# Kernel optimization log

Hardware: AMD Instinct MI355X
Metric: run time of the kernel (lower is better)

Reference implementation:

```python
import jax, jax.numpy as jnp
import numpy as np

B, N, TAPS, T = 64, 2000, 64, 2000


def setup_inputs() -> dict:
    key = jax.random.key(0)
    k1, k2 = jax.random.split(key)
    return {
        "x_seq": jax.random.normal(k1, (B, N, TAPS), dtype=jnp.float32),
        "d_seq": jax.random.normal(k2, (B, N), dtype=jnp.float32),
        # one learnable forgetting factor per unrolled RLS layer, init 0.99
        "lambdas": jnp.full((T,), 0.99, dtype=jnp.float32),
    }


def reference(x_seq, d_seq, lambdas):
    Bb, Nn, taps = x_seq.shape
    steps = min(lambdas.shape[0], Nn)
    w0 = jnp.zeros((Bb, taps), dtype=x_seq.dtype)
    P0 = jnp.broadcast_to(jnp.eye(taps, dtype=x_seq.dtype), (Bb, taps, taps))

    # time-major inputs for lax.scan
    xs = (jnp.swapaxes(x_seq[:, :steps, :], 0, 1),  # (steps, B, taps)
          jnp.swapaxes(d_seq[:, :steps], 0, 1),     # (steps, B)
          lambdas[:steps])                           # (steps,)

    def step(carry, inp):
        w, P = carry
        x, d, lam = inp
        lam = jnp.clip(lam, 1e-4, 0.9999)
        Px = jnp.einsum('bij,bj->bi', P, x)                 # (B, taps)
        denom = lam + jnp.einsum('bi,bi->b', x, Px)          # (B,)
        g = Px / denom[:, None]                              # gain (B, taps)
        y_hat = jnp.sum(w * x, axis=-1)                      # (B,)
        w_next = w + g * (d - y_hat)[:, None]
        xP = jnp.einsum('bj,bjk->bk', x, P)                  # x^T P, (B, taps)
        P_next = (P - g[:, :, None] * xP[:, None, :]) / lam  # rank-1 downdate
        return (w_next, P_next), y_hat

    (w_final, P_final), y_hats = jax.lax.scan(step, (w0, P0), xs)
    return jnp.swapaxes(y_hats, 0, 1), w_final  # (B, steps), (B, taps)
```

## Files before the change

kernel.cpp:

```cpp
#include <hip/hip_runtime.h>


#define B_ 64
#define N_ 2000
#define TAPS_ 64
#define STEPS_ 2000
#define VST_ 72

typedef float f2 __attribute__((ext_vector_type(2)));

__device__ __forceinline__ f2 pk2(float v) { f2 r; r.x = v; r.y = v; return r; }

__device__ __forceinline__ void lds_barrier() {
    asm volatile("s_waitcnt lgkmcnt(0)\n\ts_barrier" ::: "memory");
}

__device__ __forceinline__ float clipl(float v) {
    return fminf(fmaxf(v, 1e-4f), 0.9999f);
}

__device__ __forceinline__ float quad_reduce(float v) {
    float r;
    asm("s_nop 1\n\t"
        "v_add_f32_dpp %0, %1, %1 quad_perm:[1,0,3,2] row_mask:0xf bank_mask:0xf\n\t"
        "s_nop 1\n\t"
        "v_add_f32_dpp %0, %0, %0 quad_perm:[2,3,0,1] row_mask:0xf bank_mask:0xf"
        : "=&v"(r) : "v"(v));
    return r;
}

__device__ __forceinline__ float rcp_nr(float v) {
    float r = __builtin_amdgcn_rcpf(v);
    float e = fmaf(-v, r, 1.0f);
    return fmaf(r, e, r);
}

__global__ __launch_bounds__(256, 1) void rls_kernel(
    const float* __restrict__ x_seq,
    const float* __restrict__ d_seq,
    const float* __restrict__ lambdas,
    float* __restrict__ y_out,
    float* __restrict__ w_out)
{
    const int b   = blockIdx.x;
    const int tid = threadIdx.x;
    const int r   = tid >> 2;
    const int q   = tid & 3;
    const int qb  = q << 4;

    __shared__ __align__(16) float  bufs[2][4][VST_];
    __shared__ __align__(16) float  d_lds[STEPS_];
    __shared__ __align__(16) float2 lam2[STEPS_];

    const float* xb = x_seq + (size_t)b * N_ * TAPS_;
    const float* db = d_seq + (size_t)b * N_;

    for (int idx = tid; idx < STEPS_; idx += 256) {
        d_lds[idx] = db[idx];
        const float lc = clipl(lambdas[idx]);
        lam2[idx] = make_float2(lc, rcp_nr(lc));
    }

    f2 Q[8], QT[8], w[8];
    #pragma unroll
    for (int j = 0; j < 8; ++j) {
        Q[j].x = (qb + 2*j     == r) ? 1.0f : 0.0f;
        Q[j].y = (qb + 2*j + 1 == r) ? 1.0f : 0.0f;
        QT[j] = Q[j];
        w[j]  = pk2(0.0f);
    }
    float sig = 1.0f;

    auto unpack4 = [](f2* dst, float4 v) {
        dst[0].x = v.x; dst[0].y = v.y; dst[1].x = v.z; dst[1].y = v.w;
    };

    auto loadpair = [&](f2 (&dA)[8], f2 (&dB)[8], int row) {
        const float4* v0 = (const float4*)(xb + (size_t)row * TAPS_ + qb);
        const float4* v1 = (const float4*)(xb + (size_t)(row + 1) * TAPS_ + qb);
        #pragma unroll
        for (int j4 = 0; j4 < 4; ++j4) {
            unpack4(&dA[2*j4], v0[j4]);
            unpack4(&dB[2*j4], v1[j4]);
        }
    };

    f2 P0a[8], P0b[8], P1a[8], P1b[8], P2a[8], P2b[8], P3a[8], P3b[8];
    loadpair(P0a, P0b, 0);
    loadpair(P1a, P1b, 2);
    loadpair(P2a, P2b, 4);

    float qxrS, xqrS, urS, vrS, wy0S, wy1S;

    {
        f2 qx2 = pk2(0.f), xq2 = pk2(0.f), u2 = pk2(0.f), v2 = pk2(0.f);
        #pragma unroll
        for (int j = 0; j < 8; ++j) {
            qx2 = __builtin_elementwise_fma(Q[j],  P0a[j], qx2);
            xq2 = __builtin_elementwise_fma(QT[j], P0a[j], xq2);
            u2  = __builtin_elementwise_fma(Q[j],  P0b[j], u2);
            v2  = __builtin_elementwise_fma(QT[j], P0b[j], v2);
        }
        qxrS = quad_reduce(qx2.x + qx2.y);
        xqrS = quad_reduce(xq2.x + xq2.y);
        urS  = quad_reduce(u2.x + u2.y);
        vrS  = quad_reduce(v2.x + v2.y);
        bufs[0][q][r] = (q == 0) ? qxrS : (q == 1) ? xqrS : (q == 2) ? urS : vrS;

        f2 wy02 = pk2(0.f), wy12 = pk2(0.f);
        #pragma unroll
        for (int j = 0; j < 8; ++j) {
            wy02 = __builtin_elementwise_fma(w[j], P0a[j], wy02);
            wy12 = __builtin_elementwise_fma(w[j], P0b[j], wy12);
        }
        wy0S = quad_reduce(wy02.x + wy02.y);
        wy1S = quad_reduce(wy12.x + wy12.y);
    }

    auto round = [&](int t, f2 (&x0)[8], f2 (&x1)[8],
                     f2 (&xn0)[8], f2 (&xn1)[8],
                     f2 (&xf0)[8], f2 (&xf1)[8],
                     int par, bool pf, bool fuse)
    {
        lds_barrier();

        f2 Qxq[8], xQq[8], uq[8], vq[8];
        {
            const float4* p0 = (const float4*)(&bufs[par][0][qb]);
            const float4* p1 = (const float4*)(&bufs[par][1][qb]);
            #pragma unroll
            for (int j4 = 0; j4 < 4; ++j4) {
                unpack4(&Qxq[2*j4], p0[j4]);
                unpack4(&xQq[2*j4], p1[j4]);
            }
            const float4* p2 = (const float4*)(&bufs[par][2][qb]);
            const float4* p3 = (const float4*)(&bufs[par][3][qb]);
            #pragma unroll
            for (int j4 = 0; j4 < 4; ++j4) {
                unpack4(&uq[2*j4], p2[j4]);
                unpack4(&vq[2*j4], p3[j4]);
            }
        }
        const float4 lf = *(const float4*)&lam2[t];
        const float2 dd = *(const float2*)&d_lds[t];

        if (pf) loadpair(xf0, xf1, t + 6);

        f2 pd2 = pk2(0.f);
        #pragma unroll
        for (int j = 0; j < 8; ++j)
            pd2 = __builtin_elementwise_fma(x0[j], Qxq[j], pd2);
        const float pd0  = quad_reduce(pd2.x + pd2.y);
        const float den0 = fmaf(sig, pd0, lf.x);
        const float s0   = sig * rcp_nr(den0);

        f2 a2 = pk2(0.f), bb2 = pk2(0.f);
        #pragma unroll
        for (int j = 0; j < 8; ++j) {
            a2  = __builtin_elementwise_fma(x1[j], xQq[j], a2);
            bb2 = __builtin_elementwise_fma(x1[j], Qxq[j], bb2);
        }
        const float a  = quad_reduce(a2.x + a2.y);
        const float bb = quad_reduce(bb2.x + bb2.y);

        f2 c22 = pk2(0.f);
        #pragma unroll
        for (int j = 0; j < 8; ++j)
            c22 = __builtin_elementwise_fma(x1[j], uq[j], c22);
        const float c2 = quad_reduce(c22.x + c22.y);

        const float err0 = dd.x - wy0S;
        const float es0  = s0 * err0;
        const float sa   = s0 * a;
        const float sb   = s0 * bb;

        const float sig1 = sig * lf.y;
        const float pd1  = fmaf(-sa, bb, c2);
        const float den1 = fmaf(sig1, pd1, lf.z);
        const float s1   = sig1 * rcp_nr(den1);
        const float y1   = fmaf(es0, bb, wy1S);
        const float err1 = dd.y - y1;
        const float es1  = s1 * err1;
        sig = sig1 * lf.w;

        if (tid == 0)
            *(float2*)(y_out + (size_t)b * N_ + t) = make_float2(wy0S, y1);

        const float qx1r = fmaf(-sa, qxrS, urS);
        const float xq1r = fmaf(-sb, xqrS, vrS);
        const f2 nsa   = pk2(-sa);
        const f2 nsb   = pk2(-sb);
        const f2 s0v   = pk2(s0);
        const f2 s1v   = pk2(s1);
        const f2 es0v  = pk2(es0);
        const f2 es1v  = pk2(es1);
        const f2 ntr0  = pk2(-(s0 * qxrS));
        const f2 ntr1  = pk2(-(s1 * qx1r));
        const f2 nxqr  = pk2(-xqrS);
        const f2 nxq1r = pk2(-xq1r);

        f2 nqx = pk2(0.f), nxq = pk2(0.f), nu = pk2(0.f), nv = pk2(0.f);
        f2 nw0 = pk2(0.f), nw1 = pk2(0.f);

        #pragma unroll
        for (int j = 0; j < 8; ++j) {
            const f2 Qx1 = __builtin_elementwise_fma(nsa, Qxq[j], uq[j]);
            const f2 xQ1 = __builtin_elementwise_fma(nsb, xQq[j], vq[j]);
            const f2 tq0 = s0v * Qxq[j];
            const f2 tq1 = s1v * Qx1;
            w[j] = __builtin_elementwise_fma(Qxq[j], es0v, w[j]);
            w[j] = __builtin_elementwise_fma(Qx1,    es1v, w[j]);
            Q[j] = __builtin_elementwise_fma(ntr0, xQq[j], Q[j]);
            Q[j] = __builtin_elementwise_fma(ntr1, xQ1,    Q[j]);
            QT[j] = __builtin_elementwise_fma(tq0, nxqr,  QT[j]);
            QT[j] = __builtin_elementwise_fma(tq1, nxq1r, QT[j]);
            if (fuse) {
                nqx = __builtin_elementwise_fma(Q[j],  xn0[j], nqx);
                nxq = __builtin_elementwise_fma(QT[j], xn0[j], nxq);
                nu  = __builtin_elementwise_fma(Q[j],  xn1[j], nu);
                nv  = __builtin_elementwise_fma(QT[j], xn1[j], nv);
                nw0 = __builtin_elementwise_fma(w[j],  xn0[j], nw0);
                nw1 = __builtin_elementwise_fma(w[j],  xn1[j], nw1);
            }
        }

        if (fuse) {
            qxrS = quad_reduce(nqx.x + nqx.y);
            xqrS = quad_reduce(nxq.x + nxq.y);
            urS  = quad_reduce(nu.x + nu.y);
            vrS  = quad_reduce(nv.x + nv.y);
            bufs[par ^ 1][q][r] =
                (q == 0) ? qxrS : (q == 1) ? xqrS : (q == 2) ? urS : vrS;
            wy0S = quad_reduce(nw0.x + nw0.y);
            wy1S = quad_reduce(nw1.x + nw1.y);
        }
    };

    for (int t = 0; t < 1992; t += 8) {
        round(t + 0, P0a, P0b, P1a, P1b, P3a, P3b, 0, true, true);
        round(t + 2, P1a, P1b, P2a, P2b, P0a, P0b, 1, true, true);
        round(t + 4, P2a, P2b, P3a, P3b, P1a, P1b, 0, true, true);
        round(t + 6, P3a, P3b, P0a, P0b, P2a, P2b, 1, true, true);
    }
    round(1992, P0a, P0b, P1a, P1b, P3a, P3b, 0, true,  true);
    round(1994, P1a, P1b, P2a, P2b, P0a, P0b, 1, false, true);
    round(1996, P2a, P2b, P3a, P3b, P1a, P1b, 0, false, true);
    round(1998, P3a, P3b, P0a, P0b, P2a, P2b, 1, false, false);

    if (r == 0) {
        float4* wo = (float4*)(w_out + (size_t)b * TAPS_ + qb);
        #pragma unroll
        for (int j4 = 0; j4 < 4; ++j4)
            wo[j4] = make_float4(w[2*j4].x, w[2*j4].y, w[2*j4+1].x, w[2*j4+1].y);
    }
}

extern "C" void kernel_launch(void* const* d_in, const int* in_sizes, int n_in,
                              void* d_out, int out_size, void* d_ws, size_t ws_size,
                              hipStream_t stream) {
    const float* x_seq   = (const float*)d_in[0];
    const float* d_seq   = (const float*)d_in[1];
    const float* lambdas = (const float*)d_in[2];

    float* y_out = (float*)d_out;
    float* w_out = (float*)d_out + (size_t)B_ * N_;

    rls_kernel<<<B_, 256, 0, stream>>>(x_seq, d_seq, lambdas, y_out, w_out);
}
```

Measured before the change: 900.4 us.

## Block four RLS time steps per barrier round instead of two

Extends the blocked rank-update scheme from two to four steps per round. The small Gram-like dot products among the four input vectors are computed serially and the four rank-1 updates of Q, QT and w are applied together. This halves the number of LDS barriers and exchange rounds per sequence. In exchange, each round carries more serial scalar dependency work and much higher register pressure, and the prefetch distance drops to one quad ahead.

```diff
diff --git a/kernel.cpp b/kernel.cpp
--- a/kernel.cpp
+++ b/kernel.cpp
@@ -48,7 +48,7 @@
     const int q   = tid & 3;
     const int qb  = q << 4;
 
-    __shared__ __align__(16) float  bufs[2][4][VST_];
+    __shared__ __align__(16) float  bufs[2][8][VST_];
     __shared__ __align__(16) float  d_lds[STEPS_];
     __shared__ __align__(16) float2 lam2[STEPS_];
 
@@ -75,177 +75,241 @@
         dst[0].x = v.x; dst[0].y = v.y; dst[1].x = v.z; dst[1].y = v.w;
     };
 
-    auto loadpair = [&](f2 (&dA)[8], f2 (&dB)[8], int row) {
-        const float4* v0 = (const float4*)(xb + (size_t)row * TAPS_ + qb);
-        const float4* v1 = (const float4*)(xb + (size_t)(row + 1) * TAPS_ + qb);
-        #pragma unroll
-        for (int j4 = 0; j4 < 4; ++j4) {
-            unpack4(&dA[2*j4], v0[j4]);
-            unpack4(&dB[2*j4], v1[j4]);
+    f2 XA[4][8], XB[4][8];
+    auto loadquad = [&](f2 (&dst)[4][8], int row0) {
+        #pragma unroll
+        for (int i = 0; i < 4; ++i) {
+            const float4* v = (const float4*)(xb + (size_t)(row0 + i) * TAPS_ + qb);
+            #pragma unroll
+            for (int j4 = 0; j4 < 4; ++j4)
+                unpack4(&dst[i][2*j4], v[j4]);
         }
     };
-
-    f2 P0a[8], P0b[8], P1a[8], P1b[8], P2a[8], P2b[8], P3a[8], P3b[8];
-    loadpair(P0a, P0b, 0);
-    loadpair(P1a, P1b, 2);
-    loadpair(P2a, P2b, 4);
-
-    float qxrS, xqrS, urS, vrS, wy0S, wy1S;
+    loadquad(XA, 0);
+
+    float g0rS, g1rS, g2rS, g3rS, h0rS, h1rS, h2rS, h3rS;
+    float wy0S, wy1S, wy2S, wy3S;
 
     {
-        f2 qx2 = pk2(0.f), xq2 = pk2(0.f), u2 = pk2(0.f), v2 = pk2(0.f);
+        f2 cg[4], ch[4], cw[4];
+        #pragma unroll
+        for (int i = 0; i < 4; ++i) { cg[i] = pk2(0.f); ch[i] = pk2(0.f); cw[i] = pk2(0.f); }
         #pragma unroll
         for (int j = 0; j < 8; ++j) {
-            qx2 = __builtin_elementwise_fma(Q[j],  P0a[j], qx2);
-            xq2 = __builtin_elementwise_fma(QT[j], P0a[j], xq2);
-            u2  = __builtin_elementwise_fma(Q[j],  P0b[j], u2);
-            v2  = __builtin_elementwise_fma(QT[j], P0b[j], v2);
-        }
-        qxrS = quad_reduce(qx2.x + qx2.y);
-        xqrS = quad_reduce(xq2.x + xq2.y);
-        urS  = quad_reduce(u2.x + u2.y);
-        vrS  = quad_reduce(v2.x + v2.y);
-        bufs[0][q][r] = (q == 0) ? qxrS : (q == 1) ? xqrS : (q == 2) ? urS : vrS;
-
-        f2 wy02 = pk2(0.f), wy12 = pk2(0.f);
-        #pragma unroll
-        for (int j = 0; j < 8; ++j) {
-            wy02 = __builtin_elementwise_fma(w[j], P0a[j], wy02);
-            wy12 = __builtin_elementwise_fma(w[j], P0b[j], wy12);
-        }
-        wy0S = quad_reduce(wy02.x + wy02.y);
-        wy1S = quad_reduce(wy12.x + wy12.y);
-    }
-
-    auto round = [&](int t, f2 (&x0)[8], f2 (&x1)[8],
-                     f2 (&xn0)[8], f2 (&xn1)[8],
-                     f2 (&xf0)[8], f2 (&xf1)[8],
+            #pragma unroll
+            for (int i = 0; i < 4; ++i) {
+                cg[i] = __builtin_elementwise_fma(Q[j],  XA[i][j], cg[i]);
+                ch[i] = __builtin_elementwise_fma(QT[j], XA[i][j], ch[i]);
+                cw[i] = __builtin_elementwise_fma(w[j],  XA[i][j], cw[i]);
+            }
+        }
+        g0rS = quad_reduce(cg[0].x + cg[0].y);
+        g1rS = quad_reduce(cg[1].x + cg[1].y);
+        g2rS = quad_reduce(cg[2].x + cg[2].y);
+        g3rS = quad_reduce(cg[3].x + cg[3].y);
+        h0rS = quad_reduce(ch[0].x + ch[0].y);
+        h1rS = quad_reduce(ch[1].x + ch[1].y);
+        h2rS = quad_reduce(ch[2].x + ch[2].y);
+        h3rS = quad_reduce(ch[3].x + ch[3].y);
+        wy0S = quad_reduce(cw[0].x + cw[0].y);
+        wy1S = quad_reduce(cw[1].x + cw[1].y);
+        wy2S = quad_reduce(cw[2].x + cw[2].y);
+        wy3S = quad_reduce(cw[3].x + cw[3].y);
+        const float gw = (q == 0) ? g0rS : (q == 1) ? g1rS : (q == 2) ? g2rS : g3rS;
+        const float hw = (q == 0) ? h0rS : (q == 1) ? h1rS : (q == 2) ? h2rS : h3rS;
+        bufs[0][q][r]     = gw;
+        bufs[0][4 + q][r] = hw;
+    }
+
+    auto round = [&](int t, f2 (&xc)[4][8], f2 (&xn)[4][8],
                      int par, bool pf, bool fuse)
     {
         lds_barrier();
 
-        f2 Qxq[8], xQq[8], uq[8], vq[8];
-        {
-            const float4* p0 = (const float4*)(&bufs[par][0][qb]);
-            const float4* p1 = (const float4*)(&bufs[par][1][qb]);
-            #pragma unroll
-            for (int j4 = 0; j4 < 4; ++j4) {
-                unpack4(&Qxq[2*j4], p0[j4]);
-                unpack4(&xQq[2*j4], p1[j4]);
+        f2 gs[4][8], hs[4][8];
+        #pragma unroll
+        for (int v = 0; v < 4; ++v) {
+            const float4* p = (const float4*)(&bufs[par][v][qb]);
+            #pragma unroll
+            for (int j4 = 0; j4 < 4; ++j4)
+                unpack4(&gs[v][2*j4], p[j4]);
+        }
+        #pragma unroll
+        for (int v = 0; v < 4; ++v) {
+            const float4* p = (const float4*)(&bufs[par][4 + v][qb]);
+            #pragma unroll
+            for (int j4 = 0; j4 < 4; ++j4)
+                unpack4(&hs[v][2*j4], p[j4]);
+        }
+        const float4 lfA = *(const float4*)&lam2[t];
+        const float4 lfB = *(const float4*)&lam2[t + 2];
+        const float4 dd4 = *(const float4*)&d_lds[t];
+
+        if (pf) loadquad(xn, t + 4);
+
+        auto dot = [&](const f2 (&a)[8], const f2 (&s)[8]) -> float {
+            f2 acc = pk2(0.f);
+            #pragma unroll
+            for (int j = 0; j < 8; ++j)
+                acc = __builtin_elementwise_fma(a[j], s[j], acc);
+            return quad_reduce(acc.x + acc.y);
+        };
+        const float m00 = dot(xc[0], gs[0]);
+
+        const float den0 = fmaf(sig, m00, lfA.x);
+        const float sc0  = sig * rcp_nr(den0);
+        sig *= lfA.y;
+        const float e0 = sc0 * (dd4.x - wy0S);
+
+        const float m01 = dot(xc[1], gs[0]);
+        const float n01 = dot(xc[1], hs[0]);
+        const float m11 = dot(xc[1], gs[1]);
+
+        const float P01 = m01, R01 = n01;
+        const float nA01 = -(sc0 * R01), nB01 = -(sc0 * P01);
+
+        const float pd1  = fmaf(nA01, P01, m11);
+        const float den1 = fmaf(sig, pd1, lfA.z);
+        const float sc1  = sig * rcp_nr(den1);
+        sig *= lfA.w;
+        const float y1v = fmaf(e0, P01, wy1S);
+        const float e1  = sc1 * (dd4.y - y1v);
+
+        const float m02 = dot(xc[2], gs[0]);
+        const float n02 = dot(xc[2], hs[0]);
+        const float m12 = dot(xc[2], gs[1]);
+        const float n12 = dot(xc[2], hs[1]);
+        const float m22 = dot(xc[2], gs[2]);
+
+        const float P02 = m02, R02 = n02;
+        const float nA02 = -(sc0 * R02), nB02 = -(sc0 * P02);
+        const float P12 = fmaf(nA01, P02, m12);
+        const float R12 = fmaf(nB01, R02, n12);
+        const float nA12 = -(sc1 * R12), nB12 = -(sc1 * P12);
+
+        const float pd2  = fmaf(nA12, P12, fmaf(nA02, P02, m22));
+        const float den2 = fmaf(sig, pd2, lfB.x);
+        const float sc2  = sig * rcp_nr(den2);
+        sig *= lfB.y;
+        const float y2v = fmaf(e1, P12, fmaf(e0, P02, wy2S));
+        const float e2  = sc2 * (dd4.z - y2v);
+
+        const float m03 = dot(xc[3], gs[0]);
+        const float n03 = dot(xc[3], hs[0]);
+        const float m13 = dot(xc[3], gs[1]);
+        const float n13 = dot(xc[3], hs[1]);
+        const float m23 = dot(xc[3], gs[2]);
+        const float n23 = dot(xc[3], hs[2]);
+        const float m33 = dot(xc[3], gs[3]);
+
+        const float P03 = m03, R03 = n03;
+        const float nA03 = -(sc0 * R03), nB03 = -(sc0 * P03);
+        const float P13 = fmaf(nA01, P03, m13);
+        const float R13 = fmaf(nB01, R03, n13);
+        const float nA13 = -(sc1 * R13), nB13 = -(sc1 * P13);
+        const float P23 = fmaf(nA12, P13, fmaf(nA02, P03, m23));
+        const float R23 = fmaf(nB12, R13, fmaf(nB02, R03, n23));
+        const float nA23 = -(sc2 * R23), nB23 = -(sc2 * P23);
+
+        const float pd3  = fmaf(nA23, P23, fmaf(nA13, P13, fmaf(nA03, P03, m33)));
+        const float den3 = fmaf(sig, pd3, lfB.z);
+        const float sc3  = sig * rcp_nr(den3);
+        sig *= lfB.w;
+        const float y3v = fmaf(e2, P23, fmaf(e1, P13, fmaf(e0, P03, wy3S)));
+        const float e3  = sc3 * (dd4.w - y3v);
+
+        if (tid == 0)
+            *(float4*)(y_out + (size_t)b * N_ + t) =
+                make_float4(wy0S, y1v, y2v, y3v);
+
+        const float A0r = g0rS, B0r = h0rS;
+        const float A1r = fmaf(nA01, A0r, g1rS);
+        const float B1r = fmaf(nB01, B0r, h1rS);
+        float A2r = fmaf(nA02, A0r, g2rS); A2r = fmaf(nA12, A1r, A2r);
+        float B2r = fmaf(nB02, B0r, h2rS); B2r = fmaf(nB12, B1r, B2r);
+        float A3r = fmaf(nA03, A0r, g3rS); A3r = fmaf(nA13, A1r, A3r); A3r = fmaf(nA23, A2r, A3r);
+        float B3r = fmaf(nB03, B0r, h3rS); B3r = fmaf(nB13, B1r, B3r); B3r = fmaf(nB23, B2r, B3r);
+
+        const f2 nA01v = pk2(nA01), nA02v = pk2(nA02), nA03v = pk2(nA03);
+        const f2 nA12v = pk2(nA12), nA13v = pk2(nA13), nA23v = pk2(nA23);
+        const f2 nB01v = pk2(nB01), nB02v = pk2(nB02), nB03v = pk2(nB03);
+        const f2 nB12v = pk2(nB12), nB13v = pk2(nB13), nB23v = pk2(nB23);
+        const f2 e0v = pk2(e0), e1v = pk2(e1), e2v = pk2(e2), e3v = pk2(e3);
+        const f2 sc0v = pk2(sc0), sc1v = pk2(sc1), sc2v = pk2(sc2), sc3v = pk2(sc3);
+        const f2 nQ0v = pk2(-(sc0 * A0r)), nQ1v = pk2(-(sc1 * A1r));
+        const f2 nQ2v = pk2(-(sc2 * A2r)), nQ3v = pk2(-(sc3 * A3r));
+        const f2 nB0rv = pk2(-B0r), nB1rv = pk2(-B1r);
+        const f2 nB2rv = pk2(-B2r), nB3rv = pk2(-B3r);
+
+        f2 ng[4], nh[4], nw[4];
+        #pragma unroll
+        for (int i = 0; i < 4; ++i) { ng[i] = pk2(0.f); nh[i] = pk2(0.f); nw[i] = pk2(0.f); }
+
+        #pragma unroll
+        for (int j = 0; j < 8; ++j) {
+            gs[1][j] = __builtin_elementwise_fma(nA01v, gs[0][j], gs[1][j]);
+            gs[2][j] = __builtin_elementwise_fma(nA02v, gs[0][j], gs[2][j]);
+            gs[2][j] = __builtin_elementwise_fma(nA12v, gs[1][j], gs[2][j]);
+            gs[3][j] = __builtin_elementwise_fma(nA03v, gs[0][j], gs[3][j]);
+            gs[3][j] = __builtin_elementwise_fma(nA13v, gs[1][j], gs[3][j]);
+            gs[3][j] = __builtin_elementwise_fma(nA23v, gs[2][j], gs[3][j]);
+            hs[1][j] = __builtin_elementwise_fma(nB01v, hs[0][j], hs[1][j]);
+            hs[2][j] = __builtin_elementwise_fma(nB02v, hs[0][j], hs[2][j]);
+            hs[2][j] = __builtin_elementwise_fma(nB12v, hs[1][j], hs[2][j]);
+            hs[3][j] = __builtin_elementwise_fma(nB03v, hs[0][j], hs[3][j]);
+            hs[3][j] = __builtin_elementwise_fma(nB13v, hs[1][j], hs[3][j]);
+            hs[3][j] = __builtin_elementwise_fma(nB23v, hs[2][j], hs[3][j]);
+            w[j] = __builtin_elementwise_fma(gs[0][j], e0v, w[j]);
+            w[j] = __builtin_elementwise_fma(gs[1][j], e1v, w[j]);
+            w[j] = __builtin_elementwise_fma(gs[2][j], e2v, w[j]);
+            w[j] = __builtin_elementwise_fma(gs[3][j], e3v, w[j]);
+            Q[j] = __builtin_elementwise_fma(nQ0v, hs[0][j], Q[j]);
+            Q[j] = __builtin_elementwise_fma(nQ1v, hs[1][j], Q[j]);
+            Q[j] = __builtin_elementwise_fma(nQ2v, hs[2][j], Q[j]);
+            Q[j] = __builtin_elementwise_fma(nQ3v, hs[3][j], Q[j]);
+            {
+                f2 tq;
+                tq = sc0v * gs[0][j]; QT[j] = __builtin_elementwise_fma(tq, nB0rv, QT[j]);
+                tq = sc1v * gs[1][j]; QT[j] = __builtin_elementwise_fma(tq, nB1rv, QT[j]);
+                tq = sc2v * gs[2][j]; QT[j] = __builtin_elementwise_fma(tq, nB2rv, QT[j]);
+                tq = sc3v * gs[3][j]; QT[j] = __builtin_elementwise_fma(tq, nB3rv, QT[j]);
             }
-            const float4* p2 = (const float4*)(&bufs[par][2][qb]);
-            const float4* p3 = (const float4*)(&bufs[par][3][qb]);
-            #pragma unroll
-            for (int j4 = 0; j4 < 4; ++j4) {
-                unpack4(&uq[2*j4], p2[j4]);
-                unpack4(&vq[2*j4], p3[j4]);
+            if (fuse) {
+                #pragma unroll
+                for (int i = 0; i < 4; ++i) {
+                    ng[i] = __builtin_elementwise_fma(Q[j],  xn[i][j], ng[i]);
+                    nh[i] = __builtin_elementwise_fma(QT[j], xn[i][j], nh[i]);
+                    nw[i] = __builtin_elementwise_fma(w[j],  xn[i][j], nw[i]);
+                }
             }
         }
-        const float4 lf = *(const float4*)&lam2[t];
-        const float2 dd = *(const float2*)&d_lds[t];
-
-        if (pf) loadpair(xf0, xf1, t + 6);
-
-        f2 pd2 = pk2(0.f);
-        #pragma unroll
-        for (int j = 0; j < 8; ++j)
-            pd2 = __builtin_elementwise_fma(x0[j], Qxq[j], pd2);
-        const float pd0  = quad_reduce(pd2.x + pd2.y);
-        const float den0 = fmaf(sig, pd0, lf.x);
-        const float s0   = sig * rcp_nr(den0);
-
-        f2 a2 = pk2(0.f), bb2 = pk2(0.f);
-        #pragma unroll
-        for (int j = 0; j < 8; ++j) {
-            a2  = __builtin_elementwise_fma(x1[j], xQq[j], a2);
-            bb2 = __builtin_elementwise_fma(x1[j], Qxq[j], bb2);
-        }
-        const float a  = quad_reduce(a2.x + a2.y);
-        const float bb = quad_reduce(bb2.x + bb2.y);
-
-        f2 c22 = pk2(0.f);
-        #pragma unroll
-        for (int j = 0; j < 8; ++j)
-            c22 = __builtin_elementwise_fma(x1[j], uq[j], c22);
-        const float c2 = quad_reduce(c22.x + c22.y);
-
-        const float err0 = dd.x - wy0S;
-        const float es0  = s0 * err0;
-        const float sa   = s0 * a;
-        const float sb   = s0 * bb;
-
-        const float sig1 = sig * lf.y;
-        const float pd1  = fmaf(-sa, bb, c2);
-        const float den1 = fmaf(sig1, pd1, lf.z);
-        const float s1   = sig1 * rcp_nr(den1);
-        const float y1   = fmaf(es0, bb, wy1S);
-        const float err1 = dd.y - y1;
-        const float es1  = s1 * err1;
-        sig = sig1 * lf.w;
-
-        if (tid == 0)
-            *(float2*)(y_out + (size_t)b * N_ + t) = make_float2(wy0S, y1);
-
-        const float qx1r = fmaf(-sa, qxrS, urS);
-        const float xq1r = fmaf(-sb, xqrS, vrS);
-        const f2 nsa   = pk2(-sa);
-        const f2 nsb   = pk2(-sb);
-        const f2 s0v   = pk2(s0);
-        const f2 s1v   = pk2(s1);
-        const f2 es0v  = pk2(es0);
-        const f2 es1v  = pk2(es1);
-        const f2 ntr0  = pk2(-(s0 * qxrS));
-        const f2 ntr1  = pk2(-(s1 * qx1r));
-        const f2 nxqr  = pk2(-xqrS);
-        const f2 nxq1r = pk2(-xq1r);
-
-        f2 nqx = pk2(0.f), nxq = pk2(0.f), nu = pk2(0.f), nv = pk2(0.f);
-        f2 nw0 = pk2(0.f), nw1 = pk2(0.f);
-
-        #pragma unroll
-        for (int j = 0; j < 8; ++j) {
-            const f2 Qx1 = __builtin_elementwise_fma(nsa, Qxq[j], uq[j]);
-            const f2 xQ1 = __builtin_elementwise_fma(nsb, xQq[j], vq[j]);
-            const f2 tq0 = s0v * Qxq[j];
-            const f2 tq1 = s1v * Qx1;
-            w[j] = __builtin_elementwise_fma(Qxq[j], es0v, w[j]);
-            w[j] = __builtin_elementwise_fma(Qx1,    es1v, w[j]);
-            Q[j] = __builtin_elementwise_fma(ntr0, xQq[j], Q[j]);
-            Q[j] = __builtin_elementwise_fma(ntr1, xQ1,    Q[j]);
-            QT[j] = __builtin_elementwise_fma(tq0, nxqr,  QT[j]);
-            QT[j] = __builtin_elementwise_fma(tq1, nxq1r, QT[j]);
-            if (fuse) {
-                nqx = __builtin_elementwise_fma(Q[j],  xn0[j], nqx);
-                nxq = __builtin_elementwise_fma(QT[j], xn0[j], nxq);
-                nu  = __builtin_elementwise_fma(Q[j],  xn1[j], nu);
-                nv  = __builtin_elementwise_fma(QT[j], xn1[j], nv);
-                nw0 = __builtin_elementwise_fma(w[j],  xn0[j], nw0);
-                nw1 = __builtin_elementwise_fma(w[j],  xn1[j], nw1);
-            }
-        }
 
         if (fuse) {
-            qxrS = quad_reduce(nqx.x + nqx.y);
-            xqrS = quad_reduce(nxq.x + nxq.y);
-            urS  = quad_reduce(nu.x + nu.y);
-            vrS  = quad_reduce(nv.x + nv.y);
-            bufs[par ^ 1][q][r] =
-                (q == 0) ? qxrS : (q == 1) ? xqrS : (q == 2) ? urS : vrS;
-            wy0S = quad_reduce(nw0.x + nw0.y);
-            wy1S = quad_reduce(nw1.x + nw1.y);
+            g0rS = quad_reduce(ng[0].x + ng[0].y);
+            g1rS = quad_reduce(ng[1].x + ng[1].y);
+            g2rS = quad_reduce(ng[2].x + ng[2].y);
+            g3rS = quad_reduce(ng[3].x + ng[3].y);
+            h0rS = quad_reduce(nh[0].x + nh[0].y);
+            h1rS = quad_reduce(nh[1].x + nh[1].y);
+            h2rS = quad_reduce(nh[2].x + nh[2].y);
+            h3rS = quad_reduce(nh[3].x + nh[3].y);
+            const float gw = (q == 0) ? g0rS : (q == 1) ? g1rS : (q == 2) ? g2rS : g3rS;
+            const float hw = (q == 0) ? h0rS : (q == 1) ? h1rS : (q == 2) ? h2rS : h3rS;
+            bufs[par ^ 1][q][r]     = gw;
+            bufs[par ^ 1][4 + q][r] = hw;
+            wy0S = quad_reduce(nw[0].x + nw[0].y);
+            wy1S = quad_reduce(nw[1].x + nw[1].y);
+            wy2S = quad_reduce(nw[2].x + nw[2].y);
+            wy3S = quad_reduce(nw[3].x + nw[3].y);
         }
     };
 
     for (int t = 0; t < 1992; t += 8) {
-        round(t + 0, P0a, P0b, P1a, P1b, P3a, P3b, 0, true, true);
-        round(t + 2, P1a, P1b, P2a, P2b, P0a, P0b, 1, true, true);
-        round(t + 4, P2a, P2b, P3a, P3b, P1a, P1b, 0, true, true);
-        round(t + 6, P3a, P3b, P0a, P0b, P2a, P2b, 1, true, true);
-    }
-    round(1992, P0a, P0b, P1a, P1b, P3a, P3b, 0, true,  true);
-    round(1994, P1a, P1b, P2a, P2b, P0a, P0b, 1, false, true);
-    round(1996, P2a, P2b, P3a, P3b, P1a, P1b, 0, false, true);
-    round(1998, P3a, P3b, P0a, P0b, P2a, P2b, 1, false, false);
+        round(t,     XA, XB, 0, true, true);
+        round(t + 4, XB, XA, 1, true, true);
+    }
+    round(1992, XA, XB, 0, true,  true);
+    round(1996, XB, XA, 1, false, false);
 
     if (r == 0) {
         float4* wo = (float4*)(w_out + (size_t)b * TAPS_ + qb);
```

Result: slower. 1.223 ms (+35.8%).
